# Performance work log

Measured on AMD Instinct MI355X. Metric: run time of the kernel, lower is better.

## Reference

```python
import jax, jax.numpy as jnp
import numpy as np
import math

D_MODEL = 1024
N_HEADS = 16
HEAD_DIM = D_MODEL // N_HEADS
B, S = 4, 4096


def setup_inputs() -> dict:
    key = jax.random.key(0)
    ks = jax.random.split(key, 8)
    # xavier-uniform-ish scale for square DxD matrices
    lim = math.sqrt(6.0 / (D_MODEL + D_MODEL))
    def W(k):
        return jax.random.uniform(k, (D_MODEL, D_MODEL), jnp.float32, -lim, lim)
    return {
        "x": jax.random.normal(ks[0], (B, S, D_MODEL), jnp.float32),
        "fractal_dim": jnp.float32(1.7),
        "Wq": W(ks[1]), "bq": jnp.zeros((D_MODEL,), jnp.float32),
        "Wk": W(ks[2]), "bk": jnp.zeros((D_MODEL,), jnp.float32),
        "Wv": W(ks[3]), "bv": jnp.zeros((D_MODEL,), jnp.float32),
        "Wo": W(ks[4]), "bo": jnp.zeros((D_MODEL,), jnp.float32),
        "alpha": jnp.float32(1.5),
        "frac_scale": jnp.float32(0.5),
    }


def reference(x, fractal_dim, Wq, bq, Wk, bk, Wv, bv, Wo, bo, alpha, frac_scale):
    b, s, d = x.shape
    h, hd = N_HEADS, HEAD_DIM
    residual = x

    adaptive_alpha = alpha + frac_scale * (fractal_dim - 1.5)

    q = (x @ Wq + bq).reshape(b, s, h, hd)
    k = (x @ Wk + bk).reshape(b, s, h, hd)
    v = (x @ Wv + bv).reshape(b, s, h, hd)

    # spectral filter over frequency axis (seq dim)
    freqs = jnp.fft.fftfreq(s).astype(x.dtype)  # [S]
    phase = adaptive_alpha * jnp.arctan(jnp.log(jnp.abs(freqs) + 1e-10))
    filt = jnp.exp(1j * phase)[None, :, None, None]  # [1,S,1,1] complex

    def spectral(t):
        tf = jnp.fft.fft(t, axis=1, norm="ortho") * filt
        return jnp.fft.ifft(tf, axis=1, norm="ortho").real

    q_t, k_t, v_t = spectral(q), spectral(k), spectral(v)

    # per-(token) dot product across head_dim -> logits over heads
    logits = jnp.einsum("bshd,bshd->bsh", q_t, k_t) / math.sqrt(hd)
    w = jax.nn.softmax(logits, axis=-1)  # softmax over heads
    attended = w[..., None] * v_t  # [B,S,H,Hd]

    # final inverse FFT of the (real) attended signal along seq dim
    attended_time = jnp.fft.ifft(attended.astype(jnp.complex64), axis=1, norm="ortho").real

    out = attended_time.reshape(b, s, d) @ Wo + bo
    return out + residual
```

## Files before the change

kernel.cpp:

```cpp
#include <hip/hip_runtime.h>

#define S      4096
#define DM     1024
#define NB     4
#define NH     16
#define HDIM   64
#define MTOT   (NB * S)
#define DS     ((long)DM * S)
#define MH     2304
#define KH     2112
#define KH2    2112
#define MEO    2048

typedef __attribute__((ext_vector_type(8))) short short8;
typedef __attribute__((ext_vector_type(4))) float f32x4;
typedef __attribute__((ext_vector_type(8))) unsigned short u16x8;
typedef __attribute__((ext_vector_type(4))) unsigned short u16x4;

__device__ __forceinline__ unsigned short f2bf(float f) {
  union { float f; unsigned u; } v; v.f = f;
  unsigned r = v.u + 0x7fffu + ((v.u >> 16) & 1u);
  return (unsigned short)(r >> 16);
}
__device__ __forceinline__ float bf2f(short h) {
  union { unsigned u; float f; } v; v.u = ((unsigned)(unsigned short)h) << 16;
  return v.f;
}

#define GLOAD(gp, lp) __builtin_amdgcn_global_load_lds( \
    (const __attribute__((address_space(1))) void*)(gp), \
    (__attribute__((address_space(3))) void*)(lp), 16, 0, 0)

#define SBAR() do { asm volatile("" ::: "memory"); __builtin_amdgcn_s_barrier(); \
                    asm volatile("" ::: "memory"); } while (0)
#define WAITL0() asm volatile("s_waitcnt lgkmcnt(0)" ::: "memory")

#define SWZ(o) ((o) ^ ((((o) >> 7) & 3) << 4))


__global__ void k_tabg(const float* __restrict__ fd, const float* __restrict__ alpha,
                       const float* __restrict__ fsc,
                       float* __restrict__ cos_tab, float* __restrict__ c_arr,
                       float* __restrict__ g) {
  const float twopi = 6.28318530717958647692f;
  float aa = alpha[0] + fsc[0] * (fd[0] - 1.5f);
  int bx = blockIdx.x;
  if (bx < 16) {
    int k = bx * 256 + threadIdx.x;
    cos_tab[k] = cosf(twopi * ((float)k / (float)S));
    int kk = (k <= S / 2) ? k : (S - k);
    float af = (float)kk / (float)S;
    c_arr[k] = cosf(aa * atanf(logf(af + 1e-10f)));
    return;
  }
  __shared__ float sct[S];
  __shared__ float sc[S];
  __shared__ float red[16][17];
  for (int i = threadIdx.x; i < S; i += 256) {
    sct[i] = cosf(twopi * ((float)i / (float)S));
    int kk = (i <= S / 2) ? i : (S - i);
    float af = (float)kk / (float)S;
    sc[i] = cosf(aa * atanf(logf(af + 1e-10f)));
  }
  __syncthreads();
  int jl = threadIdx.x >> 4, r = threadIdx.x & 15;
  int j = (bx - 16) * 16 + jl;
  float acc = 0.f;
#pragma unroll 4
  for (int i = 0; i < 256; ++i) {
    int k = r + 16 * i;
    acc += sc[k] * sct[(j * k) & (S - 1)];
  }
  red[jl][r] = acc;
  __syncthreads();
  if (r == 0) {
    float s = 0.f;
#pragma unroll
    for (int i = 0; i < 16; ++i) s += red[jl][i];
    g[j] = s * (1.f / (float)S);
  }
}

__global__ void k_buildEO(const float* __restrict__ g, short* __restrict__ Ge) {
  long i8 = ((long)blockIdx.x * 256 + threadIdx.x) * 8;
  if (i8 >= (long)MEO * KH2) return;
  int n = (int)(i8 / KH2);
  int m = (int)(i8 % KH2);
  u16x8 ev, ov;
#pragma unroll
  for (int j = 0; j < 8; ++j) {
    int mm = m + j;
    float e, o;
    if (mm == 0)            { e = g[n]; o = 0.f; }
    else if (mm == 2048)    { e = g[(n + 2048) & (S - 1)]; o = 0.f; }
    else if (mm > 2048)     { e = 0.f; o = 0.f; }
    else {
      float a = g[(n - mm) & (S - 1)], b = g[(n + mm) & (S - 1)];
      e = 0.5f * (a + b); o = 0.5f * (a - b);
    }
    ev[j] = f2bf(e); ov[j] = f2bf(o);
  }
  *(u16x8*)(Ge + i8) = ev;
  *(u16x8*)(Ge + (long)MEO * KH2 + i8) = ov;
}

__global__ void k_prep(const float* __restrict__ x, short* __restrict__ uv,
                       const float* __restrict__ W0, const float* __restrict__ W1,
                       const float* __restrict__ W2, const float* __restrict__ W3,
                       short* __restrict__ WT) {
  __shared__ float sh[2 * 64 * 65];
  int bx = blockIdx.x, by = blockIdx.y, bz = blockIdx.z;
  int t = threadIdx.x;
  int r = t >> 4, c4 = (t & 15) * 4;
  if (bx >= 33) {
    float (*tile)[65] = (float(*)[65])sh;
    const float* W = (bz == 0) ? W0 : ((bz == 1) ? W1 : ((bz == 2) ? W2 : W3));
    short* WTo = WT + (size_t)bz * DM * DM;
    int k0 = (bx - 33) * 64, n0 = by * 64;
    const float* ip = W + (long)k0 * DM + n0;
#pragma unroll
    for (int rr = 0; rr < 4; ++rr) {
      float4 v = *(const float4*)(ip + (long)(r + rr * 16) * DM + c4);
      tile[r + rr * 16][c4 + 0] = v.x;
      tile[r + rr * 16][c4 + 1] = v.y;
      tile[r + rr * 16][c4 + 2] = v.z;
      tile[r + rr * 16][c4 + 3] = v.w;
    }
    __syncthreads();
    int k_loc = t & 63, nq = t >> 6;
    short* op = WTo + (long)n0 * DM + k0;
#pragma unroll
    for (int i = 0; i < 16; ++i) {
      int n_loc = nq * 16 + i;
      op[(long)n_loc * DM + k_loc] = (short)f2bf(tile[k_loc][n_loc]);
    }
    return;
  }
  float (*tp)[65] = (float(*)[65])sh;
  float (*tm)[65] = (float(*)[65])(sh + 64 * 65);
  int m0 = bx * 64, d0 = by * 64, b = bz;
#pragma unroll
  for (int rr = 0; rr < 4; ++rr) {
    int m = m0 + r + rr * 16;
    float4 vp = *(const float4*)(x + ((long)(b * S + m)) * DM + d0 + c4);
    int ms = (S - m) & (S - 1);
    float4 vm = *(const float4*)(x + ((long)(b * S + ms)) * DM + d0 + c4);
    tp[r + rr * 16][c4 + 0] = vp.x; tp[r + rr * 16][c4 + 1] = vp.y;
    tp[r + rr * 16][c4 + 2] = vp.z; tp[r + rr * 16][c4 + 3] = vp.w;
    tm[r + rr * 16][c4 + 0] = vm.x; tm[r + rr * 16][c4 + 1] = vm.y;
    tm[r + rr * 16][c4 + 2] = vm.z; tm[r + rr * 16][c4 + 3] = vm.w;
  }
  __syncthreads();
  int m_loc = t & 63, dq = t >> 6;
#pragma unroll
  for (int i = 0; i < 16; ++i) {
    int d_loc = dq * 16 + i;
    int m = m0 + m_loc;
    float P = tp[m_loc][d_loc], M = tm[m_loc][d_loc];
    float u, v;
    if (m == 0 || m == 2048) { u = P; v = 0.f; }
    else if (m > 2048)       { u = 0.f; v = 0.f; }
    else                     { u = P + M; v = P - M; }
    long base = ((long)(b * DM + d0 + d_loc)) * KH2 + m;
    uv[base] = (short)f2bf(u);
    uv[base + (long)4 * DM * KH2] = (short)f2bf(v);
  }
}

__global__ void k_unfold2(const short* __restrict__ AB, const float* __restrict__ g,
                          const short* __restrict__ uv, short* __restrict__ Xs) {
  __shared__ float red[256];
  int bx = blockIdx.x;
  if (bx < 4096) {
    long i8 = ((long)bx * 256 + threadIdx.x) * 8;
    int b = (int)(i8 >> 21);
    long rr = i8 & ((1L << 21) - 1);
    int n = (int)(rr >> 10);
    int d = (int)(rr & (DM - 1));
    u16x8 av = *(const u16x8*)(AB + i8);
    u16x8 bv = *(const u16x8*)(AB + ((long)4 * MEO * DM) + i8);
    u16x8 sv, dv;
#pragma unroll
    for (int j = 0; j < 8; ++j) {
      float A = bf2f((short)av[j]), B = bf2f((short)bv[j]);
      sv[j] = f2bf(A + B);
      dv[j] = f2bf(A - B);
    }
    *(u16x8*)(Xs + ((long)b * S + n) * DM + d) = sv;
    if (n > 0)
      *(u16x8*)(Xs + ((long)b * S + (S - n)) * DM + d) = dv;
  } else {
    int bd = bx - 4096;
    int b = bd >> 10, d = bd & (DM - 1);
    const short* up = uv + ((long)(b * DM + d)) * KH2;
    int t = threadIdx.x;
    float acc = 0.f;
    for (int m = t; m <= 2048; m += 256)
      acc += g[2048 - m] * bf2f(up[m]);
    red[t] = acc;
    __syncthreads();
    for (int sh = 128; sh > 0; sh >>= 1) {
      if (t < sh) red[t] += red[t + sh];
      __syncthreads();
    }
    if (t == 0) Xs[((long)b * S + 2048) * DM + d] = (short)f2bf(red[0]);
  }
}

__global__ void k_logsoft(const short* __restrict__ Q, const short* __restrict__ K,
                          float* __restrict__ w) {
  int idx = blockIdx.x * 16 + (threadIdx.x >> 4);
  int h = threadIdx.x & 15;
  const short* q = Q + (long)idx * DM + h * HDIM;
  const short* k = K + (long)idx * DM + h * HDIM;
  float acc = 0.f;
#pragma unroll
  for (int jj = 0; jj < 8; ++jj) {
    u16x8 qa = *(const u16x8*)(q + jj * 8);
    u16x8 ka = *(const u16x8*)(k + jj * 8);
#pragma unroll
    for (int l = 0; l < 8; ++l) acc += bf2f((short)qa[l]) * bf2f((short)ka[l]);
  }
  acc *= 0.125f;
  float m = acc;
#pragma unroll
  for (int d = 1; d < 16; d <<= 1) m = fmaxf(m, __shfl_xor(m, d, 16));
  float e = expf(acc - m);
  float ssum = e;
#pragma unroll
  for (int d = 1; d < 16; d <<= 1) ssum += __shfl_xor(ssum, d, 16);
  int b = idx >> 12, s = idx & (S - 1);
  w[((long)b * NH + h) * S + s] = e / ssum;
}

__global__ void k_attfoldM2(const short* __restrict__ V, const float* __restrict__ wsm,
                            short* __restrict__ A2t,
                            const float* __restrict__ cos_tab, short* __restrict__ Mc2) {
  int bx = blockIdx.x, by = blockIdx.y, bz = blockIdx.z;
  if (bx >= 33) {
    long lin = (long)(bx - 33) + 38L * (by + 16L * bz);
    long i8 = (lin * 256 + threadIdx.x) * 8;
    if (i8 >= (long)MH * KH) return;
    int n = (int)(i8 / KH);
    int m = (int)(i8 % KH);
    u16x8 mv;
#pragma unroll
    for (int j = 0; j < 8; ++j) {
      int mm = m + j;
      float vv = (mm <= 2048) ? cos_tab[(n * mm) & (S - 1)] * 0.015625f : 0.f;
      mv[j] = f2bf(vv);
    }
    *(u16x8*)(Mc2 + i8) = mv;
    return;
  }
  __shared__ float t1[64][65];
  __shared__ float t2[64][65];
  __shared__ float w1[64], w2[64];
  int m0 = bx * 64, d0 = by * 64, b = bz;
  int t = threadIdx.x;
  int h0 = d0 >> 6;
  if (t < 64) {
    int m = m0 + t;
    const float* wp = wsm + ((long)b * NH + h0) * S;
    w1[t] = wp[m & (S - 1)];
    w2[t] = wp[(S - m) & (S - 1)];
  }
  int r = t >> 4, c4 = (t & 15) * 4;
#pragma unroll
  for (int rr = 0; rr < 4; ++rr) {
    int i = r + rr * 16;
    int m = m0 + i;
    u16x4 a = *(const u16x4*)(V + ((long)(b * S + (m & (S - 1)))) * DM + d0 + c4);
    u16x4 bb = *(const u16x4*)(V + ((long)(b * S + ((S - m) & (S - 1)))) * DM + d0 + c4);
#pragma unroll
    for (int l = 0; l < 4; ++l) {
      t1[i][c4 + l] = bf2f((short)a[l]);
      t2[i][c4 + l] = bf2f((short)bb[l]);
    }
  }
  __syncthreads();
  int i_loc = t & 63, jq = t >> 6;
  int m = m0 + i_loc;
#pragma unroll
  for (int jj = 0; jj < 16; ++jj) {
    int j = jq * 16 + jj;
    float rv;
    if (m == 0 || m == 2048) rv = w1[i_loc] * t1[i_loc][j];
    else if (m < 2048)       rv = w1[i_loc] * t1[i_loc][j] + w2[i_loc] * t2[i_loc][j];
    else                     rv = 0.f;
    A2t[((long)(b * DM + d0 + j)) * KH + m] = (short)f2bf(rv);
  }
}

template <int EPI, int AMIR = 0, int ASEL = 0, int WALK = 0, int MREP = 1>
__global__ __launch_bounds__(512, 2) void gemm8(
    const short* __restrict__ A, const short* __restrict__ Bt,
    short* __restrict__ Cb, short* __restrict__ Cb2, short* __restrict__ Cb3,
    float* __restrict__ Cf,
    const float* __restrict__ bias, const float* __restrict__ bias2,
    const float* __restrict__ bias3,
    const float* __restrict__ bsc, const float* __restrict__ resid,
    int M, int N, int K, long aBatch, long bBatch, long cBatch) {
  __shared__ __align__(16) short SH[65536];
  auto Ab = [&](int buf, int ks) { return SH + (buf * 2 + ks) * 8192; };
  auto Bb = [&](int buf, int ks) { return SH + 32768 + (buf * 2 + ks) * 8192; };

  const int gx = gridDim.x, gy = gridDim.y;
  const int nwg = gx * gy * gridDim.z;
  int lin = blockIdx.x + gx * (blockIdx.y + gy * blockIdx.z);
  int swz = lin;
  if ((nwg & 7) == 0) {
    const int cpx = nwg >> 3;
    swz = (lin & 7) * cpx + (lin >> 3);
  }
  const int NTN = N >> 8;
  const int NTM = M >> 8;
  const int tid = threadIdx.x;
  const int lane = tid & 63;
  const int wid = tid >> 6;
  const int wm = wid >> 2, wn = wid & 3;

  const int o0 = tid * 16, o1 = o0 + 8192;
  const int lo0 = SWZ(o0), lo1 = SWZ(o1);
  const int srow[2] = {lo0 >> 6, lo1 >> 6};
  const int scol[2] = {(lo0 & 63) >> 1, (lo1 & 63) >> 1};

  for (int rep = 0; rep < MREP; ++rep) {
    const int wg = swz + rep * nwg;
    int ntile, mtile, bz;
    if (WALK) {
      mtile = wg % NTM;
      const int rest = wg / NTM;
      ntile = rest % NTN;
      bz = rest / NTN;
    } else {
      ntile = wg % NTN;
      const int rest = wg / NTN;
      mtile = rest % NTM;
      bz = rest / NTM;
    }

    const short* Ag = ASEL ? (A + (long)(bz >> 2) * aBatch) : (A + (long)bz * aBatch);
    const short* Bg = Bt + (long)bz * bBatch;
    const int m0 = mtile << 8, n0 = ntile << 8;

    const short* bA[2];
    const short* bB[2];
#pragma unroll
    for (int j = 0; j < 2; ++j) {
      if (AMIR) {
        int grow = m0 + srow[j];
        int b_ = grow >> 12, s_ = grow & (S - 1);
        int sm = (s_ <= 2048) ? s_ : (4096 - s_);
        bA[j] = Ag + ((long)b_ * MH + sm) * K + scol[j];
      } else {
        bA[j] = Ag + (long)(m0 + srow[j]) * K + scol[j];
      }
      bB[j] = Bg + (long)(n0 + srow[j]) * K + scol[j];
    }

    f32x4 acc[8][4];
#pragma unroll
    for (int i = 0; i < 8; ++i)
#pragma unroll
      for (int j = 0; j < 4; ++j) acc[i][j] = (f32x4){0.f, 0.f, 0.f, 0.f};

    const int NT = K >> 6;
    auto stage = [&](int h) {
      const int tau = h >> 2, q = h & 3;
      const int ks = q >> 1;
      const long k0 = (long)tau * 64 + ks * 32;
      const int dbase = (q & 1) * 65536 + (((tau & 1) << 1) + ks) * 16384;
      const short* b0 = (q & 1) ? bB[0] : bA[0];
      const short* b1 = (q & 1) ? bB[1] : bA[1];
      GLOAD(b0 + k0, (short*)((char*)SH + dbase + o0));
      GLOAD(b1 + k0, (short*)((char*)SH + dbase + o1));
    };

    if (rep > 0) SBAR();
#pragma unroll
    for (int h = 0; h < 7; ++h) stage(h);
    asm volatile("s_waitcnt vmcnt(6)" ::: "memory");
    SBAR();

    short8 bf[4];
    for (int t = 0; t < NT; ++t) {
      const int buf = t & 1;
#pragma unroll
      for (int p = 0; p < 4; ++p) {
        const int ks = p >> 1, mh = p & 1;
        short8 af[4];
        {
          const short* Ah = Ab(buf, ks);
          const int kb = (lane >> 4) * 16;
          const int r0 = wm * 128 + mh * 64 + (lane & 15);
#pragma unroll
          for (int i = 0; i < 4; ++i) {
            int byte = (r0 + i * 16) * 64 + kb;
            byte = SWZ(byte);
            af[i] = *(const short8*)((const char*)Ah + byte);
          }
          if (mh == 0) {
            const short* Bh = Bb(buf, ks);
            const int c0 = wn * 64 + (lane & 15);
#pragma unroll
            for (int j = 0; j < 4; ++j) {
              int byte = (c0 + j * 16) * 64 + kb;
              byte = SWZ(byte);
              bf[j] = *(const short8*)((const char*)Bh + byte);
            }
          }
        }
        { const int h = 4 * t + p + 7; if (h < 4 * NT) stage(h); }
        SBAR();
        WAITL0();
        __builtin_amdgcn_s_setprio(1);
#pragma unroll
        for (int i = 0; i < 4; ++i)
#pragma unroll
          for (int j = 0; j < 4; ++j)
            acc[mh * 4 + i][j] = __builtin_amdgcn_mfma_f32_16x16x32_bf16(
                af[i], bf[j], acc[mh * 4 + i][j], 0, 0, 0);
        __builtin_amdgcn_s_setprio(0);
        if (p == 3) {
          if (t < NT - 2) {
            asm volatile("s_waitcnt vmcnt(6)" ::: "memory");
          } else if (t == NT - 2) {
            asm volatile("s_waitcnt vmcnt(0)" ::: "memory");
          }
        }
        SBAR();
      }
    }

    const int rl = (lane >> 4) << 2;
#pragma unroll
    for (int f = 0; f < 8; ++f) {
      const int rbase = m0 + wm * 128 + f * 16 + rl;
#pragma unroll
      for (int j = 0; j < 4; ++j) {
        const int col = n0 + wn * 64 + j * 16 + (lane & 15);
        f32x4 a = acc[f][j];
        if constexpr (EPI == 0) {
          short* cp = Cb + (long)bz * cBatch;
#pragma unroll
          for (int r = 0; r < 4; ++r)
            cp[(long)(rbase + r) * N + col] = (short)f2bf(a[r]);
        } else if constexpr (EPI == 4) {
          const int pidx = col >> 10;
          const int dcol = col & (DM - 1);
          short* Cp = (pidx == 0) ? Cb : ((pidx == 1) ? Cb2 : Cb3);
          const float* bp = (pidx == 0) ? bias : ((pidx == 1) ? bias2 : bias3);
          const float bi = bp[dcol] * (bsc ? bsc[0] : 1.f);
#pragma unroll
          for (int r = 0; r < 4; ++r)
            Cp[(long)(rbase + r) * DM + dcol] = (short)f2bf(a[r] + bi);
        } else {
          float bi = bias[col];
#pragma unroll
          for (int r = 0; r < 4; ++r) {
            long o = (long)(rbase + r) * N + col;
            Cf[o] = a[r] + bi + resid[o];
          }
        }
      }
    }
  }
}

extern "C" void kernel_launch(void* const* d_in, const int* in_sizes, int n_in,
                              void* d_out, int out_size, void* d_ws, size_t ws_size,
                              hipStream_t stream) {
  const float* x     = (const float*)d_in[0];
  const float* fd    = (const float*)d_in[1];
  const float* Wq    = (const float*)d_in[2];
  const float* bq    = (const float*)d_in[3];
  const float* Wk    = (const float*)d_in[4];
  const float* bk    = (const float*)d_in[5];
  const float* Wv    = (const float*)d_in[6];
  const float* bv    = (const float*)d_in[7];
  const float* Wo    = (const float*)d_in[8];
  const float* bo    = (const float*)d_in[9];
  const float* alpha = (const float*)d_in[10];
  const float* fsc   = (const float*)d_in[11];
  float* out = (float*)d_out;

  char* wp = (char*)d_ws;
  auto alloc = [&](size_t bytes) {
    char* p = wp;
    wp += (bytes + 255) & ~(size_t)255;
    return p;
  };
  float* cos_tab = (float*)alloc(S * 4);
  float* c_arr   = (float*)alloc(S * 4);
  float* g       = (float*)alloc(S * 4);
  float* wsm     = (float*)alloc((size_t)NB * NH * S * 4);
  short* WTcat = (short*)alloc((size_t)4 * DM * DM * 2);
  short* WoT   = WTcat + (size_t)3 * DM * DM;
  short* slotA = (short*)alloc((size_t)NB * DS * 2);
  short* slotB = (short*)alloc((size_t)NB * DS * 2);
  short* slotC = (short*)alloc((size_t)NB * DS * 2);

  short* uv = (short*)d_out;
  short* Qn = (short*)d_out;
  short* Kn = (short*)d_out + (size_t)NB * DS;

  short* Ge  = slotB;
  short* ABout = slotA;
  short* Xs  = slotC;
  short* Vn  = slotA;
  short* Mc2 = slotB;
  short* A2t = (short*)((char*)slotB + 10u * 1024 * 1024);
  short* att_half = slotC;

  dim3 blk(256), blk8(512);

  k_tabg<<<dim3(16 + S / 16), blk, 0, stream>>>(fd, alpha, fsc, cos_tab, c_arr, g);
  k_buildEO<<<dim3((unsigned)((long)MEO * KH2 / 8 / 256)), blk, 0, stream>>>(g, Ge);
  k_prep<<<dim3(49, 16, NB), blk, 0, stream>>>(x, uv, Wq, Wk, Wv, Wo, WTcat);

  dim3 geo(DM / 256, MEO / 256, 8);
  gemm8<0, 0, 1><<<geo, blk8, 0, stream>>>(Ge, uv, ABout, nullptr, nullptr, nullptr,
                                           nullptr, nullptr, nullptr, nullptr, nullptr,
                                           MEO, DM, KH2,
                                           (long)MEO * KH2, (long)DM * KH2, (long)MEO * DM);
  k_unfold2<<<dim3(8192), blk, 0, stream>>>(ABout, g, uv, Xs);

  gemm8<4, 0, 0, 0, 3><<<dim3(256), blk8, 0, stream>>>(
      Xs, WTcat, Qn, Kn, Vn, nullptr, bq, bk, bv, c_arr, nullptr,
      MTOT, 3 * DM, DM, 0, 0, 0);

  k_logsoft<<<dim3(MTOT / 16), blk, 0, stream>>>(Qn, Kn, wsm);
  k_attfoldM2<<<dim3(33 + 38, DM / 64, NB), blk, 0, stream>>>(Vn, wsm, A2t, cos_tab, Mc2);

  dim3 ghalf(DM / 256, MH / 256, NB);
  gemm8<0><<<ghalf, blk8, 0, stream>>>(Mc2, A2t, att_half, nullptr, nullptr, nullptr,
                                       nullptr, nullptr, nullptr, nullptr, nullptr,
                                       MH, DM, KH, 0, (long)DM * KH, (long)MH * DM);

  dim3 gproj(DM / 256, MTOT / 256, 1);
  gemm8<2, 1><<<gproj, blk8, 0, stream>>>(att_half, WoT, nullptr, nullptr, nullptr, out,
                                          bo, nullptr, nullptr, nullptr, x,
                                          MTOT, DM, DM, 0, 0, 0);
}
```

Before: 389.0 us.

## Fuse per-head QK dot product into QKV GEMM epilogue via interleaved weights

Reorders the transposed Q and K weight rows so each 256-column output tile holds Q and K for two heads. The GEMM epilogue stages the tile in swizzled shared memory and computes the per-head q·k logits directly, writing only fp32 logits. Q and K are never written to global memory. A small softmax kernel then reads the logits. This removes the Q/K round trip through HBM, at the cost of extra shared-memory traffic and a synchronization in the epilogue.

```diff
diff --git a/kernel.cpp b/kernel.cpp
--- a/kernel.cpp
+++ b/kernel.cpp
@@ -107,15 +107,30 @@
 __global__ void k_prep(const float* __restrict__ x, short* __restrict__ uv,
                        const float* __restrict__ W0, const float* __restrict__ W1,
                        const float* __restrict__ W2, const float* __restrict__ W3,
-                       short* __restrict__ WT) {
+                       short* __restrict__ WT,
+                       const float* __restrict__ bq, const float* __restrict__ bk,
+                       float* __restrict__ biasI) {
   __shared__ float sh[2 * 64 * 65];
   int bx = blockIdx.x, by = blockIdx.y, bz = blockIdx.z;
   int t = threadIdx.x;
+  if (bx == 49) {
+    if (bz != 0 || by >= 8) return;
+    int o = by * 256 + t;
+    int t2 = o >> 8, r2 = o & 255;
+    int half = r2 >> 7, isK = (r2 >> 6) & 1, j = o & 63;
+    int h = t2 * 2 + half;
+    biasI[o] = (isK ? bk : bq)[h * 64 + j];
+    return;
+  }
   int r = t >> 4, c4 = (t & 15) * 4;
   if (bx >= 33) {
     float (*tile)[65] = (float(*)[65])sh;
     const float* W = (bz == 0) ? W0 : ((bz == 1) ? W1 : ((bz == 2) ? W2 : W3));
-    short* WTo = WT + (size_t)bz * DM * DM;
+    long base_row;
+    if (bz == 0)      base_row = (by >> 1) * 256 + (by & 1) * 128;
+    else if (bz == 1) base_row = (by >> 1) * 256 + (by & 1) * 128 + 64;
+    else if (bz == 2) base_row = 2048 + by * 64;
+    else              base_row = 3072 + by * 64;
     int k0 = (bx - 33) * 64, n0 = by * 64;
     const float* ip = W + (long)k0 * DM + n0;
 #pragma unroll
@@ -128,7 +143,7 @@
     }
     __syncthreads();
     int k_loc = t & 63, nq = t >> 6;
-    short* op = WTo + (long)n0 * DM + k0;
+    short* op = WT + base_row * DM + k0;
 #pragma unroll
     for (int i = 0; i < 16; ++i) {
       int n_loc = nq * 16 + i;
@@ -207,30 +222,22 @@
   }
 }
 
-__global__ void k_logsoft(const short* __restrict__ Q, const short* __restrict__ K,
-                          float* __restrict__ w) {
-  int idx = blockIdx.x * 16 + (threadIdx.x >> 4);
-  int h = threadIdx.x & 15;
-  const short* q = Q + (long)idx * DM + h * HDIM;
-  const short* k = K + (long)idx * DM + h * HDIM;
-  float acc = 0.f;
-#pragma unroll
-  for (int jj = 0; jj < 8; ++jj) {
-    u16x8 qa = *(const u16x8*)(q + jj * 8);
-    u16x8 ka = *(const u16x8*)(k + jj * 8);
-#pragma unroll
-    for (int l = 0; l < 8; ++l) acc += bf2f((short)qa[l]) * bf2f((short)ka[l]);
-  }
-  acc *= 0.125f;
-  float m = acc;
-#pragma unroll
-  for (int d = 1; d < 16; d <<= 1) m = fmaxf(m, __shfl_xor(m, d, 16));
-  float e = expf(acc - m);
-  float ssum = e;
-#pragma unroll
-  for (int d = 1; d < 16; d <<= 1) ssum += __shfl_xor(ssum, d, 16);
+__global__ void k_softw(const float* __restrict__ logits, float* __restrict__ w) {
+  int idx = blockIdx.x * 256 + threadIdx.x;
+  if (idx >= NB * S) return;
   int b = idx >> 12, s = idx & (S - 1);
-  w[((long)b * NH + h) * S + s] = e / ssum;
+  const float* lp = logits + (long)b * NH * S + s;
+  float v[NH];
+  float m = -1e30f;
+#pragma unroll
+  for (int h = 0; h < NH; ++h) { v[h] = lp[(long)h * S]; m = fmaxf(m, v[h]); }
+  float sum = 0.f;
+#pragma unroll
+  for (int h = 0; h < NH; ++h) { v[h] = expf(v[h] - m); sum += v[h]; }
+  float inv = 1.f / sum;
+  float* wp = w + (long)b * NH * S + s;
+#pragma unroll
+  for (int h = 0; h < NH; ++h) wp[(long)h * S] = v[h] * inv;
 }
 
 __global__ void k_attfoldM2(const short* __restrict__ V, const float* __restrict__ wsm,
@@ -434,33 +441,78 @@
     }
 
     const int rl = (lane >> 4) << 2;
-#pragma unroll
-    for (int f = 0; f < 8; ++f) {
-      const int rbase = m0 + wm * 128 + f * 16 + rl;
-#pragma unroll
-      for (int j = 0; j < 4; ++j) {
-        const int col = n0 + wn * 64 + j * 16 + (lane & 15);
-        f32x4 a = acc[f][j];
-        if constexpr (EPI == 0) {
-          short* cp = Cb + (long)bz * cBatch;
-#pragma unroll
-          for (int r = 0; r < 4; ++r)
-            cp[(long)(rbase + r) * N + col] = (short)f2bf(a[r]);
-        } else if constexpr (EPI == 4) {
-          const int pidx = col >> 10;
-          const int dcol = col & (DM - 1);
-          short* Cp = (pidx == 0) ? Cb : ((pidx == 1) ? Cb2 : Cb3);
-          const float* bp = (pidx == 0) ? bias : ((pidx == 1) ? bias2 : bias3);
-          const float bi = bp[dcol] * (bsc ? bsc[0] : 1.f);
-#pragma unroll
-          for (int r = 0; r < 4; ++r)
-            Cp[(long)(rbase + r) * DM + dcol] = (short)f2bf(a[r] + bi);
-        } else {
-          float bi = bias[col];
-#pragma unroll
-          for (int r = 0; r < 4; ++r) {
-            long o = (long)(rbase + r) * N + col;
-            Cf[o] = a[r] + bi + resid[o];
+    if constexpr (EPI == 5) {
+      const float sc = bsc[0];
+      if (ntile < 8) {
+#pragma unroll
+        for (int f = 0; f < 8; ++f) {
+          const int lr0 = wm * 128 + f * 16 + rl;
+#pragma unroll
+          for (int j = 0; j < 4; ++j) {
+            const int lc = wn * 64 + j * 16 + (lane & 15);
+            const float bi = bias[(ntile << 8) + lc] * sc;
+            f32x4 a = acc[f][j];
+#pragma unroll
+            for (int r = 0; r < 4; ++r) {
+              int row = lr0 + r;
+              int ad = row * 512 + lc * 2;
+              ad ^= (row & 7) << 4;
+              *(short*)((char*)SH + ad) = (short)f2bf(a[r] + bi);
+            }
+          }
+        }
+        __syncthreads();
+        const int row = tid & 255, hp = tid >> 8;
+        float dot = 0.f;
+#pragma unroll
+        for (int i = 0; i < 8; ++i) {
+          int aq = row * 512 + hp * 256 + i * 16;       aq ^= (row & 7) << 4;
+          int ak = row * 512 + hp * 256 + 128 + i * 16; ak ^= (row & 7) << 4;
+          u16x8 qv = *(u16x8*)((char*)SH + aq);
+          u16x8 kv = *(u16x8*)((char*)SH + ak);
+#pragma unroll
+          for (int l = 0; l < 8; ++l) dot += bf2f((short)qv[l]) * bf2f((short)kv[l]);
+        }
+        const int token = m0 + row;
+        const int b_ = token >> 12, s_ = token & (S - 1);
+        const int h = ntile * 2 + hp;
+        Cf[((long)b_ * NH + h) * S + s_] = dot * 0.125f;
+      } else {
+#pragma unroll
+        for (int f = 0; f < 8; ++f) {
+          const int rbase = m0 + wm * 128 + f * 16 + rl;
+#pragma unroll
+          for (int j = 0; j < 4; ++j) {
+            const int col = n0 + wn * 64 + j * 16 + (lane & 15);
+            const int dcol = col - 2048;
+            const float bi = bias3[dcol] * sc;
+            f32x4 a = acc[f][j];
+#pragma unroll
+            for (int r = 0; r < 4; ++r)
+              Cb3[(long)(rbase + r) * DM + dcol] = (short)f2bf(a[r] + bi);
+          }
+        }
+      }
+    } else {
+#pragma unroll
+      for (int f = 0; f < 8; ++f) {
+        const int rbase = m0 + wm * 128 + f * 16 + rl;
+#pragma unroll
+        for (int j = 0; j < 4; ++j) {
+          const int col = n0 + wn * 64 + j * 16 + (lane & 15);
+          f32x4 a = acc[f][j];
+          if constexpr (EPI == 0) {
+            short* cp = Cb + (long)bz * cBatch;
+#pragma unroll
+            for (int r = 0; r < 4; ++r)
+              cp[(long)(rbase + r) * N + col] = (short)f2bf(a[r]);
+          } else {
+            float bi = bias[col];
+#pragma unroll
+            for (int r = 0; r < 4; ++r) {
+              long o = (long)(rbase + r) * N + col;
+              Cf[o] = a[r] + bi + resid[o];
+            }
           }
         }
       }
@@ -494,6 +546,8 @@
   float* cos_tab = (float*)alloc(S * 4);
   float* c_arr   = (float*)alloc(S * 4);
   float* g       = (float*)alloc(S * 4);
+  float* biasI   = (float*)alloc(2048 * 4);
+  float* logits  = (float*)alloc((size_t)NB * NH * S * 4);
   float* wsm     = (float*)alloc((size_t)NB * NH * S * 4);
   short* WTcat = (short*)alloc((size_t)4 * DM * DM * 2);
   short* WoT   = WTcat + (size_t)3 * DM * DM;
@@ -502,8 +556,6 @@
   short* slotC = (short*)alloc((size_t)NB * DS * 2);
 
   short* uv = (short*)d_out;
-  short* Qn = (short*)d_out;
-  short* Kn = (short*)d_out + (size_t)NB * DS;
 
   short* Ge  = slotB;
   short* ABout = slotA;
@@ -517,7 +569,8 @@
 
   k_tabg<<<dim3(16 + S / 16), blk, 0, stream>>>(fd, alpha, fsc, cos_tab, c_arr, g);
   k_buildEO<<<dim3((unsigned)((long)MEO * KH2 / 8 / 256)), blk, 0, stream>>>(g, Ge);
-  k_prep<<<dim3(49, 16, NB), blk, 0, stream>>>(x, uv, Wq, Wk, Wv, Wo, WTcat);
+  k_prep<<<dim3(50, 16, NB), blk, 0, stream>>>(x, uv, Wq, Wk, Wv, Wo, WTcat,
+                                               bq, bk, biasI);
 
   dim3 geo(DM / 256, MEO / 256, 8);
   gemm8<0, 0, 1><<<geo, blk8, 0, stream>>>(Ge, uv, ABout, nullptr, nullptr, nullptr,
@@ -526,11 +579,11 @@
                                            (long)MEO * KH2, (long)DM * KH2, (long)MEO * DM);
   k_unfold2<<<dim3(8192), blk, 0, stream>>>(ABout, g, uv, Xs);
 
-  gemm8<4, 0, 0, 0, 3><<<dim3(256), blk8, 0, stream>>>(
-      Xs, WTcat, Qn, Kn, Vn, nullptr, bq, bk, bv, c_arr, nullptr,
+  gemm8<5, 0, 0, 0, 3><<<dim3(256), blk8, 0, stream>>>(
+      Xs, WTcat, nullptr, nullptr, Vn, logits, biasI, nullptr, bv, c_arr, nullptr,
       MTOT, 3 * DM, DM, 0, 0, 0);
 
-  k_logsoft<<<dim3(MTOT / 16), blk, 0, stream>>>(Qn, Kn, wsm);
+  k_softw<<<dim3(NB * S / 256), blk, 0, stream>>>(logits, wsm);
   k_attfoldM2<<<dim3(33 + 38, DM / 64, NB), blk, 0, stream>>>(Vn, wsm, A2t, cos_tab, Mc2);
 
   dim3 ghalf(DM / 256, MH / 256, NB);
```

New measurement: 436.9 us. +12.3%, slower.

## Pipeline persistent QKV GEMM across tiles and fuse buildEO into prep kernel

Applied to the files above, without the earlier changes.

The persistent multi-tile QKV GEMM now runs one global load pipeline across all of its output tiles. Loads for the next tile are issued while the current tile is still being computed, which removes the drain and refill bubble at each tile boundary. Separately, the k_buildEO kernel is merged into k_prep as extra blocks, saving one launch and letting the two independent jobs run at the same time. The risks are extra register pressure from holding two tiles' pointer sets and a harder barrier and LDS buffer reuse schedule across tile boundaries.

```diff
diff --git a/kernel.cpp b/kernel.cpp
--- a/kernel.cpp
+++ b/kernel.cpp
@@ -81,36 +81,38 @@
   }
 }
 
-__global__ void k_buildEO(const float* __restrict__ g, short* __restrict__ Ge) {
-  long i8 = ((long)blockIdx.x * 256 + threadIdx.x) * 8;
-  if (i8 >= (long)MEO * KH2) return;
-  int n = (int)(i8 / KH2);
-  int m = (int)(i8 % KH2);
-  u16x8 ev, ov;
-#pragma unroll
-  for (int j = 0; j < 8; ++j) {
-    int mm = m + j;
-    float e, o;
-    if (mm == 0)            { e = g[n]; o = 0.f; }
-    else if (mm == 2048)    { e = g[(n + 2048) & (S - 1)]; o = 0.f; }
-    else if (mm > 2048)     { e = 0.f; o = 0.f; }
-    else {
-      float a = g[(n - mm) & (S - 1)], b = g[(n + mm) & (S - 1)];
-      e = 0.5f * (a + b); o = 0.5f * (a - b);
-    }
-    ev[j] = f2bf(e); ov[j] = f2bf(o);
-  }
-  *(u16x8*)(Ge + i8) = ev;
-  *(u16x8*)(Ge + (long)MEO * KH2 + i8) = ov;
-}
-
 __global__ void k_prep(const float* __restrict__ x, short* __restrict__ uv,
                        const float* __restrict__ W0, const float* __restrict__ W1,
                        const float* __restrict__ W2, const float* __restrict__ W3,
-                       short* __restrict__ WT) {
+                       short* __restrict__ WT,
+                       const float* __restrict__ g, short* __restrict__ Ge) {
   __shared__ float sh[2 * 64 * 65];
   int bx = blockIdx.x, by = blockIdx.y, bz = blockIdx.z;
   int t = threadIdx.x;
+  if (bx >= 49) {
+    long lin = (long)(bx - 49) + 54L * (by + 16L * bz);
+    long i8 = (lin * 256 + t) * 8;
+    if (i8 >= (long)MEO * KH2) return;
+    int n = (int)(i8 / KH2);
+    int m = (int)(i8 % KH2);
+    u16x8 ev, ov;
+#pragma unroll
+    for (int j = 0; j < 8; ++j) {
+      int mm = m + j;
+      float e, o;
+      if (mm == 0)            { e = g[n]; o = 0.f; }
+      else if (mm == 2048)    { e = g[(n + 2048) & (S - 1)]; o = 0.f; }
+      else if (mm > 2048)     { e = 0.f; o = 0.f; }
+      else {
+        float a = g[(n - mm) & (S - 1)], b = g[(n + mm) & (S - 1)];
+        e = 0.5f * (a + b); o = 0.5f * (a - b);
+      }
+      ev[j] = f2bf(e); ov[j] = f2bf(o);
+    }
+    *(u16x8*)(Ge + i8) = ev;
+    *(u16x8*)(Ge + (long)MEO * KH2 + i8) = ov;
+    return;
+  }
   int r = t >> 4, c4 = (t & 15) * 4;
   if (bx >= 33) {
     float (*tile)[65] = (float(*)[65])sh;
@@ -292,7 +294,7 @@
   }
 }
 
-template <int EPI, int AMIR = 0, int ASEL = 0, int WALK = 0, int MREP = 1>
+template <int EPI, int AMIR = 0, int ASEL = 0, int WALK = 0, int MREP = 1, int KNT = 0>
 __global__ __launch_bounds__(512, 2) void gemm8(
     const short* __restrict__ A, const short* __restrict__ Bt,
     short* __restrict__ Cb, short* __restrict__ Cb2, short* __restrict__ Cb3,
@@ -325,20 +327,155 @@
   const int srow[2] = {lo0 >> 6, lo1 >> 6};
   const int scol[2] = {(lo0 & 63) >> 1, (lo1 & 63) >> 1};
 
-  for (int rep = 0; rep < MREP; ++rep) {
-    const int wg = swz + rep * nwg;
+  auto decode = [&](int wg, int& mt, int& nt2, int& bzz) {
+    if (WALK) {
+      mt = wg % NTM;
+      const int rest = wg / NTM;
+      nt2 = rest % NTN;
+      bzz = rest / NTN;
+    } else {
+      nt2 = wg % NTN;
+      const int rest = wg / NTN;
+      mt = rest % NTM;
+      bzz = rest / NTM;
+    }
+  };
+
+  auto ldsReads = [&](int buf, int ks, int mh, short8 af[4], short8 bf[4]) {
+    const short* Ah = Ab(buf, ks);
+    const int kb = (lane >> 4) * 16;
+    const int r0 = wm * 128 + mh * 64 + (lane & 15);
+#pragma unroll
+    for (int i = 0; i < 4; ++i) {
+      int byte = (r0 + i * 16) * 64 + kb;
+      byte = SWZ(byte);
+      af[i] = *(const short8*)((const char*)Ah + byte);
+    }
+    if (mh == 0) {
+      const short* Bh = Bb(buf, ks);
+      const int c0 = wn * 64 + (lane & 15);
+#pragma unroll
+      for (int j = 0; j < 4; ++j) {
+        int byte = (c0 + j * 16) * 64 + kb;
+        byte = SWZ(byte);
+        bf[j] = *(const short8*)((const char*)Bh + byte);
+      }
+    }
+  };
+
+  if constexpr (MREP > 1) {
+    constexpr int LNT = (KNT == 16) ? 4 : ((KNT == 32) ? 5 : 6);
+    const int TOT = KNT * MREP;
+    int mt_[2], nt_[2];
+    const short* bA_[2][2];
+    const short* bB_[2][2];
+    auto setSlot = [&](int r) {
+      const int slot = r & 1;
+      int mt, nt2, bzz;
+      decode(swz + r * nwg, mt, nt2, bzz);
+      mt_[slot] = mt; nt_[slot] = nt2;
+      const short* Ag = ASEL ? (A + (long)(bzz >> 2) * aBatch) : (A + (long)bzz * aBatch);
+      const short* Bg = Bt + (long)bzz * bBatch;
+      const int m0 = mt << 8, n0 = nt2 << 8;
+#pragma unroll
+      for (int j = 0; j < 2; ++j) {
+        if (AMIR) {
+          int grow = m0 + srow[j];
+          int b_ = grow >> 12, s_ = grow & (S - 1);
+          int sm = (s_ <= 2048) ? s_ : (4096 - s_);
+          bA_[slot][j] = Ag + ((long)b_ * MH + sm) * K + scol[j];
+        } else {
+          bA_[slot][j] = Ag + (long)(m0 + srow[j]) * K + scol[j];
+        }
+        bB_[slot][j] = Bg + (long)(n0 + srow[j]) * K + scol[j];
+      }
+    };
+    setSlot(0);
+    setSlot(1);
+
+    auto stageG = [&](int H) {
+      const int tau = H >> 2, q = H & 3, ks = q >> 1;
+      const int slot = (tau >> LNT) & 1;
+      const int lt = tau & (KNT - 1);
+      const long k0 = (long)lt * 64 + ks * 32;
+      const int dbase = (q & 1) * 65536 + (((tau & 1) << 1) + ks) * 16384;
+      const short* b0 = (q & 1) ? bB_[slot][0] : bA_[slot][0];
+      const short* b1 = (q & 1) ? bB_[slot][1] : bA_[slot][1];
+      GLOAD(b0 + k0, (short*)((char*)SH + dbase + o0));
+      GLOAD(b1 + k0, (short*)((char*)SH + dbase + o1));
+    };
+
+#pragma unroll
+    for (int h = 0; h < 7; ++h) stageG(h);
+    asm volatile("s_waitcnt vmcnt(6)" ::: "memory");
+    SBAR();
+
+    for (int rep = 0; rep < MREP; ++rep) {
+      if (rep >= 1 && rep + 1 < MREP) setSlot(rep + 1);
+      f32x4 acc[8][4];
+#pragma unroll
+      for (int i = 0; i < 8; ++i)
+#pragma unroll
+        for (int j = 0; j < 4; ++j) acc[i][j] = (f32x4){0.f, 0.f, 0.f, 0.f};
+
+      short8 bf[4];
+      for (int t = 0; t < KNT; ++t) {
+        const int gt = rep * KNT + t;
+        const int buf = gt & 1;
+#pragma unroll
+        for (int p = 0; p < 4; ++p) {
+          const int ks = p >> 1, mh = p & 1;
+          short8 af[4];
+          ldsReads(buf, ks, mh, af, bf);
+          { const int H = 4 * gt + p + 7; if (H < 4 * TOT) stageG(H); }
+          SBAR();
+          WAITL0();
+          __builtin_amdgcn_s_setprio(1);
+#pragma unroll
+          for (int i = 0; i < 4; ++i)
+#pragma unroll
+            for (int j = 0; j < 4; ++j)
+              acc[mh * 4 + i][j] = __builtin_amdgcn_mfma_f32_16x16x32_bf16(
+                  af[i], bf[j], acc[mh * 4 + i][j], 0, 0, 0);
+          __builtin_amdgcn_s_setprio(0);
+          if (p == 3) {
+            if (gt < TOT - 2) {
+              asm volatile("s_waitcnt vmcnt(6)" ::: "memory");
+            } else if (gt == TOT - 2) {
+              asm volatile("s_waitcnt vmcnt(0)" ::: "memory");
+            }
+          }
+          SBAR();
+        }
+      }
+
+      const int m0 = mt_[rep & 1] << 8, n0 = nt_[rep & 1] << 8;
+      const int rl = (lane >> 4) << 2;
+      const float sc = bsc ? bsc[0] : 1.f;
+#pragma unroll
+      for (int f = 0; f < 8; ++f) {
+        const int rbase = m0 + wm * 128 + f * 16 + rl;
+#pragma unroll
+        for (int j = 0; j < 4; ++j) {
+          const int col = n0 + wn * 64 + j * 16 + (lane & 15);
+          f32x4 a = acc[f][j];
+          const int pidx = col >> 10;
+          const int dcol = col & (DM - 1);
+          short* Cp = (pidx == 0) ? Cb : ((pidx == 1) ? Cb2 : Cb3);
+          const float* bp = (pidx == 0) ? bias : ((pidx == 1) ? bias2 : bias3);
+          const float bi = bp[dcol] * sc;
+#pragma unroll
+          for (int r = 0; r < 4; ++r)
+            Cp[(long)(rbase + r) * DM + dcol] = (short)f2bf(a[r] + bi);
+        }
+      }
+    }
+    return;
+  }
+
+  {
     int ntile, mtile, bz;
-    if (WALK) {
-      mtile = wg % NTM;
-      const int rest = wg / NTM;
-      ntile = rest % NTN;
-      bz = rest / NTN;
-    } else {
-      ntile = wg % NTN;
-      const int rest = wg / NTN;
-      mtile = rest % NTM;
-      bz = rest / NTM;
-    }
+    decode(swz, mtile, ntile, bz);
 
     const short* Ag = ASEL ? (A + (long)(bz >> 2) * aBatch) : (A + (long)bz * aBatch);
     const short* Bg = Bt + (long)bz * bBatch;
@@ -377,7 +514,6 @@
       GLOAD(b1 + k0, (short*)((char*)SH + dbase + o1));
     };
 
-    if (rep > 0) SBAR();
 #pragma unroll
     for (int h = 0; h < 7; ++h) stage(h);
     asm volatile("s_waitcnt vmcnt(6)" ::: "memory");
@@ -390,27 +526,7 @@
       for (int p = 0; p < 4; ++p) {
         const int ks = p >> 1, mh = p & 1;
         short8 af[4];
-        {
-          const short* Ah = Ab(buf, ks);
-          const int kb = (lane >> 4) * 16;
-          const int r0 = wm * 128 + mh * 64 + (lane & 15);
-#pragma unroll
-          for (int i = 0; i < 4; ++i) {
-            int byte = (r0 + i * 16) * 64 + kb;
-            byte = SWZ(byte);
-            af[i] = *(const short8*)((const char*)Ah + byte);
-          }
-          if (mh == 0) {
-            const short* Bh = Bb(buf, ks);
-            const int c0 = wn * 64 + (lane & 15);
-#pragma unroll
-            for (int j = 0; j < 4; ++j) {
-              int byte = (c0 + j * 16) * 64 + kb;
-              byte = SWZ(byte);
-              bf[j] = *(const short8*)((const char*)Bh + byte);
-            }
-          }
-        }
+        ldsReads(buf, ks, mh, af, bf);
         { const int h = 4 * t + p + 7; if (h < 4 * NT) stage(h); }
         SBAR();
         WAITL0();
@@ -516,8 +632,7 @@
   dim3 blk(256), blk8(512);
 
   k_tabg<<<dim3(16 + S / 16), blk, 0, stream>>>(fd, alpha, fsc, cos_tab, c_arr, g);
-  k_buildEO<<<dim3((unsigned)((long)MEO * KH2 / 8 / 256)), blk, 0, stream>>>(g, Ge);
-  k_prep<<<dim3(49, 16, NB), blk, 0, stream>>>(x, uv, Wq, Wk, Wv, Wo, WTcat);
+  k_prep<<<dim3(49 + 54, 16, NB), blk, 0, stream>>>(x, uv, Wq, Wk, Wv, Wo, WTcat, g, Ge);
 
   dim3 geo(DM / 256, MEO / 256, 8);
   gemm8<0, 0, 1><<<geo, blk8, 0, stream>>>(Ge, uv, ABout, nullptr, nullptr, nullptr,
@@ -526,7 +641,7 @@
                                            (long)MEO * KH2, (long)DM * KH2, (long)MEO * DM);
   k_unfold2<<<dim3(8192), blk, 0, stream>>>(ABout, g, uv, Xs);
 
-  gemm8<4, 0, 0, 0, 3><<<dim3(256), blk8, 0, stream>>>(
+  gemm8<4, 0, 0, 0, 3, 16><<<dim3(256), blk8, 0, stream>>>(
       Xs, WTcat, Qn, Kn, Vn, nullptr, bq, bk, bv, c_arr, nullptr,
       MTOT, 3 * DM, DM, 0, 0, 0);
 
```

Measured after the change: 398.4 us. 1.02x slower.

## Fuse even/odd Toeplitz build into prep kernel and use 128x128 GEMM for attention fold

Applied to the files above, without the earlier changes.

Merges the k_buildEO work into k_prep as extra blocks, removing one launch and letting the two independent kernels overlap. Replaces the 256x256-tile, 512-thread GEMM for the attention fold (M=2304, N=1024, K=2112, batch 4) with a new 128x128-tile, 256-thread kernel that pipelines its global-to-LDS loads seven stages deep. The smaller tiles give more workgroups on a small problem, which should fill the GPU better. The cost is lower per-tile reuse and more total global traffic.

```diff
diff --git a/kernel.cpp b/kernel.cpp
--- a/kernel.cpp
+++ b/kernel.cpp
@@ -81,36 +81,38 @@
   }
 }
 
-__global__ void k_buildEO(const float* __restrict__ g, short* __restrict__ Ge) {
-  long i8 = ((long)blockIdx.x * 256 + threadIdx.x) * 8;
-  if (i8 >= (long)MEO * KH2) return;
-  int n = (int)(i8 / KH2);
-  int m = (int)(i8 % KH2);
-  u16x8 ev, ov;
-#pragma unroll
-  for (int j = 0; j < 8; ++j) {
-    int mm = m + j;
-    float e, o;
-    if (mm == 0)            { e = g[n]; o = 0.f; }
-    else if (mm == 2048)    { e = g[(n + 2048) & (S - 1)]; o = 0.f; }
-    else if (mm > 2048)     { e = 0.f; o = 0.f; }
-    else {
-      float a = g[(n - mm) & (S - 1)], b = g[(n + mm) & (S - 1)];
-      e = 0.5f * (a + b); o = 0.5f * (a - b);
-    }
-    ev[j] = f2bf(e); ov[j] = f2bf(o);
-  }
-  *(u16x8*)(Ge + i8) = ev;
-  *(u16x8*)(Ge + (long)MEO * KH2 + i8) = ov;
-}
-
 __global__ void k_prep(const float* __restrict__ x, short* __restrict__ uv,
                        const float* __restrict__ W0, const float* __restrict__ W1,
                        const float* __restrict__ W2, const float* __restrict__ W3,
-                       short* __restrict__ WT) {
+                       short* __restrict__ WT,
+                       const float* __restrict__ g, short* __restrict__ Ge) {
   __shared__ float sh[2 * 64 * 65];
   int bx = blockIdx.x, by = blockIdx.y, bz = blockIdx.z;
   int t = threadIdx.x;
+  if (bx >= 49) {
+    long lin = (long)(bx - 49) + 54L * (by + 16L * bz);
+    long i8 = (lin * 256 + t) * 8;
+    if (i8 >= (long)MEO * KH2) return;
+    int n = (int)(i8 / KH2);
+    int m = (int)(i8 % KH2);
+    u16x8 ev, ov;
+#pragma unroll
+    for (int j = 0; j < 8; ++j) {
+      int mm = m + j;
+      float e, o;
+      if (mm == 0)            { e = g[n]; o = 0.f; }
+      else if (mm == 2048)    { e = g[(n + 2048) & (S - 1)]; o = 0.f; }
+      else if (mm > 2048)     { e = 0.f; o = 0.f; }
+      else {
+        float a = g[(n - mm) & (S - 1)], b = g[(n + mm) & (S - 1)];
+        e = 0.5f * (a + b); o = 0.5f * (a - b);
+      }
+      ev[j] = f2bf(e); ov[j] = f2bf(o);
+    }
+    *(u16x8*)(Ge + i8) = ev;
+    *(u16x8*)(Ge + (long)MEO * KH2 + i8) = ov;
+    return;
+  }
   int r = t >> 4, c4 = (t & 15) * 4;
   if (bx >= 33) {
     float (*tile)[65] = (float(*)[65])sh;
@@ -468,6 +470,139 @@
   }
 }
 
+__global__ __launch_bounds__(256, 2) void gemm4(
+    const short* __restrict__ A, const short* __restrict__ Bt,
+    short* __restrict__ Cb,
+    int M, int N, int K, long bBatch, long cBatch) {
+  __shared__ __align__(16) short SH[32768];
+  auto Ab = [&](int buf, int ks) { return SH + (buf * 2 + ks) * 4096; };
+  auto Bb = [&](int buf, int ks) { return SH + 16384 + (buf * 2 + ks) * 4096; };
+
+  const int gx = gridDim.x, gy = gridDim.y;
+  const int nwg = gx * gy * gridDim.z;
+  int lin = blockIdx.x + gx * (blockIdx.y + gy * blockIdx.z);
+  int swz = lin;
+  if ((nwg & 7) == 0) {
+    const int cpx = nwg >> 3;
+    swz = (lin & 7) * cpx + (lin >> 3);
+  }
+  const int NTN = N >> 7;
+  const int NTM = M >> 7;
+  const int ntile = swz % NTN;
+  const int rest = swz / NTN;
+  const int mtile = rest % NTM;
+  const int bz = rest / NTM;
+
+  const short* Ag = A;
+  const short* Bg = Bt + (long)bz * bBatch;
+  const int m0 = mtile << 7, n0 = ntile << 7;
+  const int tid = threadIdx.x;
+  const int lane = tid & 63;
+  const int wid = tid >> 6;
+  const int wm = wid >> 1, wn = wid & 1;
+
+  const int o0 = tid * 16, o1 = o0 + 4096;
+  const int lo0 = SWZ(o0), lo1 = SWZ(o1);
+  const int srow[2] = {lo0 >> 6, lo1 >> 6};
+  const int scol[2] = {(lo0 & 63) >> 1, (lo1 & 63) >> 1};
+
+  const short* bA[2];
+  const short* bB[2];
+#pragma unroll
+  for (int j = 0; j < 2; ++j) {
+    bA[j] = Ag + (long)(m0 + srow[j]) * K + scol[j];
+    bB[j] = Bg + (long)(n0 + srow[j]) * K + scol[j];
+  }
+
+  f32x4 acc[4][4];
+#pragma unroll
+  for (int i = 0; i < 4; ++i)
+#pragma unroll
+    for (int j = 0; j < 4; ++j) acc[i][j] = (f32x4){0.f, 0.f, 0.f, 0.f};
+
+  const int NT = K >> 6;
+  auto stage = [&](int h) {
+    const int tau = h >> 2, q = h & 3;
+    const int ks = q >> 1;
+    const long k0 = (long)tau * 64 + ks * 32;
+    const int dbase = (q & 1) * 32768 + (((tau & 1) << 1) + ks) * 8192;
+    const short* b0 = (q & 1) ? bB[0] : bA[0];
+    const short* b1 = (q & 1) ? bB[1] : bA[1];
+    GLOAD(b0 + k0, (short*)((char*)SH + dbase + o0));
+    GLOAD(b1 + k0, (short*)((char*)SH + dbase + o1));
+  };
+
+#pragma unroll
+  for (int h = 0; h < 7; ++h) stage(h);
+  asm volatile("s_waitcnt vmcnt(6)" ::: "memory");
+  SBAR();
+
+  short8 bf[4];
+  for (int t = 0; t < NT; ++t) {
+    const int buf = t & 1;
+#pragma unroll
+    for (int p = 0; p < 4; ++p) {
+      const int ks = p >> 1, mh = p & 1;
+      short8 af[2];
+      {
+        const short* Ah = Ab(buf, ks);
+        const int kb = (lane >> 4) * 16;
+        const int r0 = wm * 64 + mh * 32 + (lane & 15);
+#pragma unroll
+        for (int i = 0; i < 2; ++i) {
+          int byte = (r0 + i * 16) * 64 + kb;
+          byte = SWZ(byte);
+          af[i] = *(const short8*)((const char*)Ah + byte);
+        }
+        if (mh == 0) {
+          const short* Bh = Bb(buf, ks);
+          const int c0 = wn * 64 + (lane & 15);
+#pragma unroll
+          for (int j = 0; j < 4; ++j) {
+            int byte = (c0 + j * 16) * 64 + kb;
+            byte = SWZ(byte);
+            bf[j] = *(const short8*)((const char*)Bh + byte);
+          }
+        }
+      }
+      { const int h = 4 * t + p + 7; if (h < 4 * NT) stage(h); }
+      SBAR();
+      WAITL0();
+      __builtin_amdgcn_s_setprio(1);
+#pragma unroll
+      for (int i = 0; i < 2; ++i)
+#pragma unroll
+        for (int j = 0; j < 4; ++j)
+          acc[mh * 2 + i][j] = __builtin_amdgcn_mfma_f32_16x16x32_bf16(
+              af[i], bf[j], acc[mh * 2 + i][j], 0, 0, 0);
+      __builtin_amdgcn_s_setprio(0);
+      if (p == 3) {
+        if (t < NT - 2) {
+          asm volatile("s_waitcnt vmcnt(6)" ::: "memory");
+        } else if (t == NT - 2) {
+          asm volatile("s_waitcnt vmcnt(0)" ::: "memory");
+        }
+      }
+      SBAR();
+    }
+  }
+
+  const int rl = (lane >> 4) << 2;
+  short* cp = Cb + (long)bz * cBatch;
+#pragma unroll
+  for (int f = 0; f < 4; ++f) {
+    const int rbase = m0 + wm * 64 + f * 16 + rl;
+#pragma unroll
+    for (int j = 0; j < 4; ++j) {
+      const int col = n0 + wn * 64 + j * 16 + (lane & 15);
+      f32x4 a = acc[f][j];
+#pragma unroll
+      for (int r = 0; r < 4; ++r)
+        cp[(long)(rbase + r) * N + col] = (short)f2bf(a[r]);
+    }
+  }
+}
+
 extern "C" void kernel_launch(void* const* d_in, const int* in_sizes, int n_in,
                               void* d_out, int out_size, void* d_ws, size_t ws_size,
                               hipStream_t stream) {
@@ -516,8 +651,7 @@
   dim3 blk(256), blk8(512);
 
   k_tabg<<<dim3(16 + S / 16), blk, 0, stream>>>(fd, alpha, fsc, cos_tab, c_arr, g);
-  k_buildEO<<<dim3((unsigned)((long)MEO * KH2 / 8 / 256)), blk, 0, stream>>>(g, Ge);
-  k_prep<<<dim3(49, 16, NB), blk, 0, stream>>>(x, uv, Wq, Wk, Wv, Wo, WTcat);
+  k_prep<<<dim3(49 + 54, 16, NB), blk, 0, stream>>>(x, uv, Wq, Wk, Wv, Wo, WTcat, g, Ge);
 
   dim3 geo(DM / 256, MEO / 256, 8);
   gemm8<0, 0, 1><<<geo, blk8, 0, stream>>>(Ge, uv, ABout, nullptr, nullptr, nullptr,
@@ -533,10 +667,9 @@
   k_logsoft<<<dim3(MTOT / 16), blk, 0, stream>>>(Qn, Kn, wsm);
   k_attfoldM2<<<dim3(33 + 38, DM / 64, NB), blk, 0, stream>>>(Vn, wsm, A2t, cos_tab, Mc2);
 
-  dim3 ghalf(DM / 256, MH / 256, NB);
-  gemm8<0><<<ghalf, blk8, 0, stream>>>(Mc2, A2t, att_half, nullptr, nullptr, nullptr,
-                                       nullptr, nullptr, nullptr, nullptr, nullptr,
-                                       MH, DM, KH, 0, (long)DM * KH, (long)MH * DM);
+  dim3 ghalf(DM / 128, MH / 128, NB);
+  gemm4<<<ghalf, blk, 0, stream>>>(Mc2, A2t, att_half,
+                                   MH, DM, KH, (long)DM * KH, (long)MH * DM);
 
   dim3 gproj(DM / 256, MTOT / 256, 1);
   gemm8<2, 1><<<gproj, blk8, 0, stream>>>(att_half, WoT, nullptr, nullptr, nullptr, out,
```

Result: no change. 386.6 us (-0.6%).
